# Kernel tuning notes

Measured on AMD Instinct MI355X. Metric: run time of the kernel, lower is better.

## Reference

```python
import jax, jax.numpy as jnp
import numpy as np

T, B, I, H, O = 1024, 64, 256, 512, 5

def setup_inputs() -> dict:
    key = jax.random.key(0)
    ks = jax.random.split(key, 7)
    s_ih = 1.0 / np.sqrt(H)
    return {
        "inputs": jax.random.normal(ks[0], (T, B, I), dtype=jnp.float32),
        "W_ih": jax.random.uniform(ks[1], (4 * H, I), minval=-s_ih, maxval=s_ih, dtype=jnp.float32),
        "W_hh": jax.random.uniform(ks[2], (4 * H, H), minval=-s_ih, maxval=s_ih, dtype=jnp.float32),
        "b_ih": jax.random.uniform(ks[3], (4 * H,), minval=-s_ih, maxval=s_ih, dtype=jnp.float32),
        "b_hh": jax.random.uniform(ks[4], (4 * H,), minval=-s_ih, maxval=s_ih, dtype=jnp.float32),
        "fc_w": jax.random.uniform(ks[5], (O, H), minval=-s_ih, maxval=s_ih, dtype=jnp.float32),
        "fc_b": jax.random.uniform(ks[6], (O,), minval=-s_ih, maxval=s_ih, dtype=jnp.float32),
    }

def _lstm_step(carry, x_t, W_ih, W_hh, b_ih, b_hh):
    h, c = carry
    # gates: [B, 4H]
    gates = x_t @ W_ih.T + b_ih + h @ W_hh.T + b_hh
    i_g, f_g, g_g, o_g = jnp.split(gates, 4, axis=-1)
    i_g = jax.nn.sigmoid(i_g)
    f_g = jax.nn.sigmoid(f_g)
    g_g = jnp.tanh(g_g)
    o_g = jax.nn.sigmoid(o_g)
    c_new = f_g * c + i_g * g_g
    h_new = o_g * jnp.tanh(c_new)
    return (h_new, c_new), h_new

def reference(inputs, W_ih, W_hh, b_ih, b_hh, fc_w, fc_b):
    batch = inputs.shape[1]
    h0 = jnp.zeros((batch, H), dtype=inputs.dtype)
    c0 = jnp.zeros((batch, H), dtype=inputs.dtype)
    step = lambda carry, x_t: _lstm_step(carry, x_t, W_ih, W_hh, b_ih, b_hh)
    (h_T, c_T), hs = jax.lax.scan(step, (h0, c0), inputs)  # hs: [T, B, H]
    outputs = hs @ fc_w.T + fc_b  # [T, B, O]
    return outputs, (h_T, c_T)
```

## Files before the change

### kernel.cpp

```cpp
#include <hip/hip_runtime.h>
#include <stdint.h>

#define T_ 1024
#define B_ 64
#define I_ 256
#define H_ 512
#define O_ 5
#define NCHAIN 8
#define NB 8
#define JW 16
#define GRID_MAIN 256
#define BLOCK_MAIN 256
#define XBS 264
#define EX_OFF 4096
#define BH (B_*H_)
#define TBO (T_*B_*O_)
#define POISON 0x7F7F7F7Fu

typedef __bf16 bf16x8 __attribute__((ext_vector_type(8)));
typedef float floatx4 __attribute__((ext_vector_type(4)));
typedef unsigned short u16;
typedef unsigned short u16x8 __attribute__((ext_vector_type(8)));
typedef unsigned int u32;
typedef u32 u32x4 __attribute__((ext_vector_type(4)));

__device__ __forceinline__ u16 f2bf(float f) {
  unsigned int u = __float_as_uint(f);
  u += 0x7fffu + ((u >> 16) & 1u);
  return (u16)(u >> 16);
}
__device__ __forceinline__ float bf2f(u16 v) {
  return __uint_as_float(((unsigned int)v) << 16);
}
__device__ __forceinline__ float sigmoid_f(float x) {
  return 1.0f / (1.0f + __expf(-x));
}
__device__ __forceinline__ float tanh_f(float x) {
  return 2.0f / (1.0f + __expf(-2.0f * x)) - 1.0f;
}

__device__ __forceinline__ void store_u32_l3(u32* p, u32 v) {
  asm volatile("global_store_dword %0, %1, off sc0 sc1" :: "v"(p), "v"(v) : "memory");
}

__device__ __forceinline__ void load_h4_l3(const u16* p, u32x4* r) {
  asm volatile(
    "global_load_dwordx4 %0, %4, off sc0 sc1\n\t"
    "global_load_dwordx4 %1, %4, off offset:64 sc0 sc1\n\t"
    "global_load_dwordx4 %2, %4, off offset:128 sc0 sc1\n\t"
    "global_load_dwordx4 %3, %4, off offset:192 sc0 sc1\n\t"
    "s_waitcnt vmcnt(0)"
    : "=&v"(r[0]), "=&v"(r[1]), "=&v"(r[2]), "=&v"(r[3]) : "v"(p) : "memory");
}
__device__ __forceinline__ void load_h6_l3(const u16* p, u32x4* r) {
  asm volatile(
    "global_load_dwordx4 %0, %6, off sc0 sc1\n\t"
    "global_load_dwordx4 %1, %6, off offset:64 sc0 sc1\n\t"
    "global_load_dwordx4 %2, %6, off offset:128 sc0 sc1\n\t"
    "global_load_dwordx4 %3, %6, off offset:192 sc0 sc1\n\t"
    "global_load_dwordx4 %4, %6, off offset:256 sc0 sc1\n\t"
    "global_load_dwordx4 %5, %6, off offset:320 sc0 sc1\n\t"
    "s_waitcnt vmcnt(0)"
    : "=&v"(r[0]), "=&v"(r[1]), "=&v"(r[2]), "=&v"(r[3]), "=&v"(r[4]), "=&v"(r[5])
    : "v"(p) : "memory");
}

__device__ __forceinline__ void barrier_lds() {
  asm volatile("s_waitcnt lgkmcnt(0)\n\ts_barrier" ::: "memory");
}

__device__ __forceinline__ void stage_x(const float* __restrict__ xsrc,
                                        u16 (*xb)[XBS], int u) {
  #pragma unroll
  for (int i = 0; i < 2; ++i) {
    int cid = u + 128 * i;
    int b  = cid >> 5;
    int ko = (cid & 31) * 8;
    const float4* s = (const float4*)(xsrc + (size_t)b * I_ + ko);
    float4 f0 = s[0], f1 = s[1];
    u16x8 uu;
    uu[0]=f2bf(f0.x); uu[1]=f2bf(f0.y); uu[2]=f2bf(f0.z); uu[3]=f2bf(f0.w);
    uu[4]=f2bf(f1.x); uu[5]=f2bf(f1.y); uu[6]=f2bf(f1.z); uu[7]=f2bf(f1.w);
    *(u16x8*)&xb[b][ko] = uu;
  }
}

__global__ __launch_bounds__(BLOCK_MAIN, 1)
void lstm_persistent(const float* __restrict__ x,
                     const float* __restrict__ W_ih,
                     const float* __restrict__ W_hh,
                     const float* __restrict__ b_ih,
                     const float* __restrict__ b_hh,
                     float* __restrict__ out,
                     u16* __restrict__ hist)
{
  __shared__ __align__(16) u16 xbuf[2][NB][XBS];
  __shared__ float part[4 * 4 * 16 * 17];

  const int tid  = threadIdx.x;
  const int wg   = blockIdx.x;
  const int w    = tid >> 6;
  const int lane = tid & 63;
  const int q    = lane >> 4;
  const int n    = lane & 15;
  const int chain = wg & 7;
  const int jslot = wg >> 3;
  const int jbase = jslot * JW;
  const int bbase = chain * NB;

  bf16x8 afrag[4][6];
  #pragma unroll
  for (int g = 0; g < 4; ++g) {
    #pragma unroll
    for (int kk = 0; kk < 6; ++kk) {
      const int kc  = w * 6 + kk;
      const int row = g * H_ + jbase + n;
      const float* src;
      if (kc < 8) src = W_ih + (size_t)row * I_ + kc * 32 + q * 8;
      else        src = W_hh + (size_t)row * H_ + (kc - 8) * 32 + q * 8;
      float4 f0 = ((const float4*)src)[0];
      float4 f1 = ((const float4*)src)[1];
      bf16x8 a;
      a[0]=(__bf16)f0.x; a[1]=(__bf16)f0.y; a[2]=(__bf16)f0.z; a[3]=(__bf16)f0.w;
      a[4]=(__bf16)f1.x; a[5]=(__bf16)f1.y; a[6]=(__bf16)f1.z; a[7]=(__bf16)f1.w;
      afrag[g][kk] = a;
    }
  }

  const int eb = tid >> 4;
  const int ej = tid & 15;
  float bias[4];
  float cval = 0.0f;
  if (tid < 128) {
    #pragma unroll
    for (int g = 0; g < 4; ++g)
      bias[g] = b_ih[g * H_ + jbase + ej] + b_hh[g * H_ + jbase + ej];
  }

  const int nx   = (w == 0) ? 6 : ((w == 1) ? 2 : 0);
  const int hoff = (w == 2) ? 128 : ((w == 3) ? 320 : 0);

  if (tid >= 128) stage_x(x + (size_t)bbase * I_, xbuf[0], tid - 128);
  __syncthreads();

  for (int t = 0; t < T_; ++t) {
    const int sr = t & 1, sw = (t + 1) & 1;

    bf16x8 bfrag[6];
    #pragma unroll
    for (int kk = 0; kk < 6; ++kk)
      if (kk < nx)
        bfrag[kk] = __builtin_bit_cast(bf16x8,
            *(const uint4*)&xbuf[sr][n & 7][(w * 6 + kk) * 32 + q * 8]);

    if (w > 0) {
      const u16* hp = hist + (size_t)t * BH + (size_t)(bbase + (n & 7)) * H_ +
                      hoff + q * 8;
      if (w == 1) {
        u32x4 r[4];
        for (;;) {
          load_h4_l3(hp, r);
          u32 bad = 0;
          #pragma unroll
          for (int i = 0; i < 4; ++i)
            #pragma unroll
            for (int jj = 0; jj < 4; ++jj) bad |= (r[i][jj] == POISON);
          if (!__any((int)bad)) break;
        }
        #pragma unroll
        for (int i = 0; i < 4; ++i)
          bfrag[2 + i] = __builtin_bit_cast(bf16x8, r[i]);
      } else {
        u32x4 r[6];
        for (;;) {
          load_h6_l3(hp, r);
          u32 bad = 0;
          #pragma unroll
          for (int i = 0; i < 6; ++i)
            #pragma unroll
            for (int jj = 0; jj < 4; ++jj) bad |= (r[i][jj] == POISON);
          if (!__any((int)bad)) break;
        }
        #pragma unroll
        for (int i = 0; i < 6; ++i)
          bfrag[i] = __builtin_bit_cast(bf16x8, r[i]);
      }
    }

    floatx4 acc[4] = {};
    #pragma unroll
    for (int kk = 0; kk < 6; ++kk) {
      #pragma unroll
      for (int g = 0; g < 4; ++g)
        acc[g] = __builtin_amdgcn_mfma_f32_16x16x32_bf16(afrag[g][kk], bfrag[kk], acc[g], 0, 0, 0);
    }

    #pragma unroll
    for (int g = 0; g < 4; ++g)
      #pragma unroll
      for (int r = 0; r < 4; ++r)
        part[((w * 4 + g) * 16 + (q * 4 + r)) * 17 + n] = acc[g][r];
    barrier_lds();

    if (tid < 128) {
      float gate[4];
      #pragma unroll
      for (int g = 0; g < 4; ++g) {
        float s = bias[g];
        #pragma unroll
        for (int w2 = 0; w2 < 4; ++w2)
          s += part[((w2 * 4 + g) * 16 + ej) * 17 + eb];
        gate[g] = s;
      }
      const float ig = sigmoid_f(gate[0]);
      const float fg = sigmoid_f(gate[1]);
      const float gg = tanh_f(gate[2]);
      const float og = sigmoid_f(gate[3]);
      cval = fg * cval + ig * gg;
      const float hval = og * tanh_f(cval);
      const int bg = bbase + eb;
      const int jg = jbase + ej;
      const u32 hb = (u32)f2bf(hval);
      const u32 other = __shfl_xor((int)hb, 1, 64);
      if ((tid & 1) == 0) {
        const u32 packed = hb | (other << 16);
        store_u32_l3((u32*)(hist + (size_t)(t + 1) * BH + (size_t)bg * H_ + jg), packed);
      }
      if (t == T_ - 1) {
        out[TBO + (size_t)bg * H_ + jg]      = hval;
        out[TBO + BH + (size_t)bg * H_ + jg] = cval;
      }
    } else {
      const int ts = (t + 1 < T_) ? (t + 1) : (T_ - 1);
      stage_x(x + ((size_t)ts * B_ + bbase) * I_, xbuf[sw], tid - 128);
    }
    barrier_lds();
  }
}

__global__ __launch_bounds__(256)
void fc_kernel(const u16* __restrict__ hist,
               const float* __restrict__ fc_w,
               const float* __restrict__ fc_b,
               float* __restrict__ out)
{
  const int gw   = (blockIdx.x * 256 + threadIdx.x) >> 6;
  const int lane = threadIdx.x & 63;
  const int t = gw >> 6;
  const int b = gw & 63;
  const u16* hrow = hist + ((size_t)(t + 1) * B_ + b) * H_ + lane * 8;
  uint4 hv = *(const uint4*)hrow;
  float h[8];
  {
    u16x8 hu = __builtin_bit_cast(u16x8, hv);
    #pragma unroll
    for (int i = 0; i < 8; ++i) h[i] = bf2f(hu[i]);
  }
  float accs[O_];
  #pragma unroll
  for (int o = 0; o < O_; ++o) {
    const float* wr = fc_w + (size_t)o * H_ + lane * 8;
    float4 w0 = ((const float4*)wr)[0];
    float4 w1 = ((const float4*)wr)[1];
    accs[o] = h[0]*w0.x + h[1]*w0.y + h[2]*w0.z + h[3]*w0.w
            + h[4]*w1.x + h[5]*w1.y + h[6]*w1.z + h[7]*w1.w;
  }
  #pragma unroll
  for (int o = 0; o < O_; ++o)
    #pragma unroll
    for (int off = 32; off > 0; off >>= 1)
      accs[o] += __shfl_down(accs[o], off, 64);
  if (lane == 0) {
    #pragma unroll
    for (int o = 0; o < O_; ++o)
      out[((size_t)t * B_ + b) * O_ + o] = accs[o] + fc_b[o];
  }
}

extern "C" void kernel_launch(void* const* d_in, const int* in_sizes, int n_in,
                              void* d_out, int out_size, void* d_ws, size_t ws_size,
                              hipStream_t stream)
{
  (void)in_sizes; (void)n_in; (void)out_size; (void)ws_size;
  const float* x    = (const float*)d_in[0];
  const float* W_ih = (const float*)d_in[1];
  const float* W_hh = (const float*)d_in[2];
  const float* b_ih = (const float*)d_in[3];
  const float* b_hh = (const float*)d_in[4];
  const float* fc_w = (const float*)d_in[5];
  const float* fc_b = (const float*)d_in[6];
  float* out = (float*)d_out;

  u16* hist = (u16*)((char*)d_ws + EX_OFF);

  hipMemsetAsync(d_ws, 0, EX_OFF + (size_t)BH * 2, stream);
  hipMemsetAsync((char*)d_ws + EX_OFF + (size_t)BH * 2, 0x7F,
                 (size_t)T_ * BH * 2, stream);

  lstm_persistent<<<GRID_MAIN, BLOCK_MAIN, 0, stream>>>(
      x, W_ih, W_hh, b_ih, b_hh, out, hist);
  fc_kernel<<<(T_ * B_) / 4, 256, 0, stream>>>(hist, fc_w, fc_b, out);
}
```

Measured before the change: 2.103 ms.

## Repartition persistent LSTM into 64 larger blocks with all-thread gate epilogue and x prefetch

```diff
diff --git a/kernel.cpp b/kernel.cpp
--- a/kernel.cpp
+++ b/kernel.cpp
@@ -6,12 +6,13 @@
 #define I_ 256
 #define H_ 512
 #define O_ 5
-#define NCHAIN 8
-#define NB 8
-#define JW 16
-#define GRID_MAIN 256
-#define BLOCK_MAIN 256
+#define NCHAIN 4
+#define NB 16
+#define JW 32
+#define GRID_MAIN 64
+#define BLOCK_MAIN 512
 #define XBS 264
+#define PS 18
 #define EX_OFF 4096
 #define BH (B_*H_)
 #define TBO (T_*B_*O_)
@@ -69,22 +70,6 @@
   asm volatile("s_waitcnt lgkmcnt(0)\n\ts_barrier" ::: "memory");
 }
 
-__device__ __forceinline__ void stage_x(const float* __restrict__ xsrc,
-                                        u16 (*xb)[XBS], int u) {
-  #pragma unroll
-  for (int i = 0; i < 2; ++i) {
-    int cid = u + 128 * i;
-    int b  = cid >> 5;
-    int ko = (cid & 31) * 8;
-    const float4* s = (const float4*)(xsrc + (size_t)b * I_ + ko);
-    float4 f0 = s[0], f1 = s[1];
-    u16x8 uu;
-    uu[0]=f2bf(f0.x); uu[1]=f2bf(f0.y); uu[2]=f2bf(f0.z); uu[3]=f2bf(f0.w);
-    uu[4]=f2bf(f1.x); uu[5]=f2bf(f1.y); uu[6]=f2bf(f1.z); uu[7]=f2bf(f1.w);
-    *(u16x8*)&xb[b][ko] = uu;
-  }
-}
-
 __global__ __launch_bounds__(BLOCK_MAIN, 1)
 void lstm_persistent(const float* __restrict__ x,
                      const float* __restrict__ W_ih,
@@ -95,7 +80,7 @@
                      u16* __restrict__ hist)
 {
   __shared__ __align__(16) u16 xbuf[2][NB][XBS];
-  __shared__ float part[4 * 4 * 16 * 17];
+  __shared__ float part[4 * 8 * 16 * PS];
 
   const int tid  = threadIdx.x;
   const int wg   = blockIdx.x;
@@ -103,60 +88,78 @@
   const int lane = tid & 63;
   const int q    = lane >> 4;
   const int n    = lane & 15;
-  const int chain = wg & 7;
-  const int jslot = wg >> 3;
+  const int kq   = w & 3;
+  const int mg   = w >> 2;
+  const int chain = wg & 3;
+  const int jslot = wg >> 2;
   const int jbase = jslot * JW;
   const int bbase = chain * NB;
 
-  bf16x8 afrag[4][6];
+  bf16x8 afrag[2][2][6];
   #pragma unroll
-  for (int g = 0; g < 4; ++g) {
-    #pragma unroll
-    for (int kk = 0; kk < 6; ++kk) {
-      const int kc  = w * 6 + kk;
-      const int row = g * H_ + jbase + n;
-      const float* src;
-      if (kc < 8) src = W_ih + (size_t)row * I_ + kc * 32 + q * 8;
-      else        src = W_hh + (size_t)row * H_ + (kc - 8) * 32 + q * 8;
-      float4 f0 = ((const float4*)src)[0];
-      float4 f1 = ((const float4*)src)[1];
-      bf16x8 a;
-      a[0]=(__bf16)f0.x; a[1]=(__bf16)f0.y; a[2]=(__bf16)f0.z; a[3]=(__bf16)f0.w;
-      a[4]=(__bf16)f1.x; a[5]=(__bf16)f1.y; a[6]=(__bf16)f1.z; a[7]=(__bf16)f1.w;
-      afrag[g][kk] = a;
-    }
-  }
-
-  const int eb = tid >> 4;
-  const int ej = tid & 15;
+  for (int gp = 0; gp < 2; ++gp) {
+    #pragma unroll
+    for (int jt = 0; jt < 2; ++jt) {
+      const int row = (2 * mg + gp) * H_ + jbase + jt * 16 + n;
+      #pragma unroll
+      for (int kk = 0; kk < 6; ++kk) {
+        const int kc = kq * 6 + kk;
+        const float* src;
+        if (kc < 8) src = W_ih + (size_t)row * I_ + kc * 32 + q * 8;
+        else        src = W_hh + (size_t)row * H_ + (kc - 8) * 32 + q * 8;
+        float4 f0 = ((const float4*)src)[0];
+        float4 f1 = ((const float4*)src)[1];
+        bf16x8 a;
+        a[0]=(__bf16)f0.x; a[1]=(__bf16)f0.y; a[2]=(__bf16)f0.z; a[3]=(__bf16)f0.w;
+        a[4]=(__bf16)f1.x; a[5]=(__bf16)f1.y; a[6]=(__bf16)f1.z; a[7]=(__bf16)f1.w;
+        afrag[gp][jt][kk] = a;
+      }
+    }
+  }
+
+  const int rj = tid >> 4;
+  const int rn = tid & 15;
+  const int jt_r = rj >> 4, jr = rj & 15;
   float bias[4];
+  #pragma unroll
+  for (int g = 0; g < 4; ++g)
+    bias[g] = b_ih[g * H_ + jbase + rj] + b_hh[g * H_ + jbase + rj];
   float cval = 0.0f;
-  if (tid < 128) {
-    #pragma unroll
-    for (int g = 0; g < 4; ++g)
-      bias[g] = b_ih[g * H_ + jbase + ej] + b_hh[g * H_ + jbase + ej];
-  }
-
-  const int nx   = (w == 0) ? 6 : ((w == 1) ? 2 : 0);
-  const int hoff = (w == 2) ? 128 : ((w == 3) ? 320 : 0);
-
-  if (tid >= 128) stage_x(x + (size_t)bbase * I_, xbuf[0], tid - 128);
+
+  const int nx   = (kq == 0) ? 6 : ((kq == 1) ? 2 : 0);
+  const int hoff = (kq == 2) ? 128 : ((kq == 3) ? 320 : 0);
+
+  const int sb  = tid >> 5;
+  const int sko = (tid & 31) * 8;
+  float4 px[2];
+
+  {
+    const float* s0 = x + ((size_t)bbase + sb) * I_ + sko;
+    float4 f0 = ((const float4*)s0)[0], f1 = ((const float4*)s0)[1];
+    u16x8 uu;
+    uu[0]=f2bf(f0.x); uu[1]=f2bf(f0.y); uu[2]=f2bf(f0.z); uu[3]=f2bf(f0.w);
+    uu[4]=f2bf(f1.x); uu[5]=f2bf(f1.y); uu[6]=f2bf(f1.z); uu[7]=f2bf(f1.w);
+    *(u16x8*)&xbuf[0][sb][sko] = uu;
+    const float* s1 = x + ((size_t)B_ + bbase + sb) * I_ + sko;
+    px[0] = ((const float4*)s1)[0];
+    px[1] = ((const float4*)s1)[1];
+  }
   __syncthreads();
 
   for (int t = 0; t < T_; ++t) {
-    const int sr = t & 1, sw = (t + 1) & 1;
+    const int sr = t & 1, sw = sr ^ 1;
 
     bf16x8 bfrag[6];
     #pragma unroll
     for (int kk = 0; kk < 6; ++kk)
       if (kk < nx)
         bfrag[kk] = __builtin_bit_cast(bf16x8,
-            *(const uint4*)&xbuf[sr][n & 7][(w * 6 + kk) * 32 + q * 8]);
-
-    if (w > 0) {
-      const u16* hp = hist + (size_t)t * BH + (size_t)(bbase + (n & 7)) * H_ +
+            *(const uint4*)&xbuf[sr][n][(kq * 6 + kk) * 32 + q * 8]);
+
+    if (kq > 0) {
+      const u16* hp = hist + (size_t)t * BH + (size_t)(bbase + n) * H_ +
                       hoff + q * 8;
-      if (w == 1) {
+      if (kq == 1) {
         u32x4 r[4];
         for (;;) {
           load_h4_l3(hp, r);
@@ -187,52 +190,65 @@
       }
     }
 
-    floatx4 acc[4] = {};
+    floatx4 acc[2][2] = {};
     #pragma unroll
     for (int kk = 0; kk < 6; ++kk) {
       #pragma unroll
-      for (int g = 0; g < 4; ++g)
-        acc[g] = __builtin_amdgcn_mfma_f32_16x16x32_bf16(afrag[g][kk], bfrag[kk], acc[g], 0, 0, 0);
-    }
-
-    #pragma unroll
-    for (int g = 0; g < 4; ++g)
+      for (int gp = 0; gp < 2; ++gp)
+        #pragma unroll
+        for (int jt = 0; jt < 2; ++jt)
+          acc[gp][jt] = __builtin_amdgcn_mfma_f32_16x16x32_bf16(
+              afrag[gp][jt][kk], bfrag[kk], acc[gp][jt], 0, 0, 0);
+    }
+
+    #pragma unroll
+    for (int gp = 0; gp < 2; ++gp)
       #pragma unroll
-      for (int r = 0; r < 4; ++r)
-        part[((w * 4 + g) * 16 + (q * 4 + r)) * 17 + n] = acc[g][r];
+      for (int jt = 0; jt < 2; ++jt)
+        #pragma unroll
+        for (int r = 0; r < 4; ++r)
+          part[((kq * 8 + (2 * mg + gp) * 2 + jt) * 16 + q * 4 + r) * PS + n]
+              = acc[gp][jt][r];
     barrier_lds();
 
-    if (tid < 128) {
-      float gate[4];
+    float gate[4];
+    #pragma unroll
+    for (int g = 0; g < 4; ++g) {
+      float s = bias[g];
       #pragma unroll
-      for (int g = 0; g < 4; ++g) {
-        float s = bias[g];
-        #pragma unroll
-        for (int w2 = 0; w2 < 4; ++w2)
-          s += part[((w2 * 4 + g) * 16 + ej) * 17 + eb];
-        gate[g] = s;
-      }
-      const float ig = sigmoid_f(gate[0]);
-      const float fg = sigmoid_f(gate[1]);
-      const float gg = tanh_f(gate[2]);
-      const float og = sigmoid_f(gate[3]);
-      cval = fg * cval + ig * gg;
-      const float hval = og * tanh_f(cval);
-      const int bg = bbase + eb;
-      const int jg = jbase + ej;
-      const u32 hb = (u32)f2bf(hval);
-      const u32 other = __shfl_xor((int)hb, 1, 64);
-      if ((tid & 1) == 0) {
-        const u32 packed = hb | (other << 16);
-        store_u32_l3((u32*)(hist + (size_t)(t + 1) * BH + (size_t)bg * H_ + jg), packed);
-      }
-      if (t == T_ - 1) {
-        out[TBO + (size_t)bg * H_ + jg]      = hval;
-        out[TBO + BH + (size_t)bg * H_ + jg] = cval;
-      }
-    } else {
-      const int ts = (t + 1 < T_) ? (t + 1) : (T_ - 1);
-      stage_x(x + ((size_t)ts * B_ + bbase) * I_, xbuf[sw], tid - 128);
+      for (int k2 = 0; k2 < 4; ++k2)
+        s += part[((k2 * 8 + g * 2 + jt_r) * 16 + jr) * PS + rn];
+      gate[g] = s;
+    }
+    const float ig = sigmoid_f(gate[0]);
+    const float fg = sigmoid_f(gate[1]);
+    const float gg = tanh_f(gate[2]);
+    const float og = sigmoid_f(gate[3]);
+    cval = fg * cval + ig * gg;
+    const float hval = og * tanh_f(cval);
+
+    const u32 hb = (u32)f2bf(hval);
+    const u32 other = (u32)__shfl_xor((int)hb, 16, 64);
+    if ((rj & 1) == 0) {
+      const u32 packed = hb | (other << 16);
+      store_u32_l3((u32*)(hist + (size_t)(t + 1) * BH +
+                          (size_t)(bbase + rn) * H_ + jbase + rj), packed);
+    }
+    if (t == T_ - 1) {
+      out[TBO + (size_t)(bbase + rn) * H_ + jbase + rj]      = hval;
+      out[TBO + BH + (size_t)(bbase + rn) * H_ + jbase + rj] = cval;
+    }
+
+    {
+      u16x8 uu;
+      const float4 f0 = px[0], f1 = px[1];
+      uu[0]=f2bf(f0.x); uu[1]=f2bf(f0.y); uu[2]=f2bf(f0.z); uu[3]=f2bf(f0.w);
+      uu[4]=f2bf(f1.x); uu[5]=f2bf(f1.y); uu[6]=f2bf(f1.z); uu[7]=f2bf(f1.w);
+      *(u16x8*)&xbuf[sw][sb][sko] = uu;
+      const int ts2 = (t + 2 < T_) ? (t + 2) : (T_ - 1);
+      const float* s = x + ((size_t)ts2 * B_ + bbase + sb) * I_ + sko;
+      px[0] = ((const float4*)s)[0];
+      px[1] = ((const float4*)s)[1];
     }
     barrier_lds();
   }
@@ -293,7 +309,7 @@
 
   u16* hist = (u16*)((char*)d_ws + EX_OFF);
 
-  hipMemsetAsync(d_ws, 0, EX_OFF + (size_t)BH * 2, stream);
+  hipMemsetAsync((char*)d_ws + EX_OFF, 0, (size_t)BH * 2, stream);
   hipMemsetAsync((char*)d_ws + EX_OFF + (size_t)BH * 2, 0x7F,
                  (size_t)T_ * BH * 2, stream);
 
```

New measurement: 3.088 ms. +46.8%, slower.
